# Kernel optimization log

Measured on AMD Instinct MI355X. Metric: run time of the kernel, lower is better.

The kernel has to match this reference:

```python
import jax, jax.numpy as jnp
import numpy as np
from jax import lax

T, H, W, HID, K = 128, 128, 128, 32, 3
DN = ('NCDHW', 'OIDHW', 'NCDHW')


def conv3dc(x, w, b=None, squeeze=False):
    # Conv3dC: 3D conv, kernel KxKxK, 'SAME' padding; return_squeezed drops channel dim
    y = lax.conv_general_dilated(x, w, (1, 1, 1), 'SAME', dimension_numbers=DN)
    if b is not None:
        y = y + b.reshape(1, -1, 1, 1, 1)
    if squeeze:
        y = jnp.squeeze(y, 1)
    return y


def setup_inputs() -> dict:
    key = jax.random.key(0)
    ks = jax.random.split(key, 10)
    X = jax.random.normal(ks[0], (1, T, H, W), dtype=jnp.float32)
    U = jax.random.normal(ks[1], (H * W, 1), dtype=jnp.float32) * 0.01
    V = jax.random.normal(ks[2], (1, T), dtype=jnp.float32) * 0.01
    M = jax.random.uniform(ks[3], (1, 1, T, H, W), dtype=jnp.float32)
    convM_w = jax.random.normal(ks[4], (HID, 1, K, K, K), dtype=jnp.float32) * 0.05
    conv0_w = jax.random.normal(ks[5], (1, HID, K, K, K), dtype=jnp.float32) * 0.05
    conv0_b = jnp.zeros((1,), dtype=jnp.float32)
    conv1_w = jax.random.normal(ks[6], (1, HID, K, K, K), dtype=jnp.float32) * 0.05
    conv2_w = jax.random.normal(ks[7], (HID, 1, K, K, K), dtype=jnp.float32) * 0.05
    conv4_w = jax.random.normal(ks[8], (1, HID, K, K, K), dtype=jnp.float32) * 0.05
    return {
        'X': X, 'U': U, 'V': V, 'M': M,
        'convM_w': convM_w, 'conv0_w': conv0_w, 'conv0_b': conv0_b,
        'conv1_w': conv1_w, 'conv2_w': conv2_w, 'conv4_w': conv4_w,
        'tau_s_raw': jnp.float32(1.0),
        'mask_scaling': jnp.float32(5.0),
        'g': jnp.ones((HID,), dtype=jnp.float32),
        'th': jnp.full((128,), 1.8, dtype=jnp.float32),
        'g2': jnp.ones((H,), dtype=jnp.float32),
        'u_learn2': jnp.ones((5,), dtype=jnp.float32),
        'v_learn2': jnp.ones((5,), dtype=jnp.float32),
    }


def reference(X, U, V, M, convM_w, conv0_w, conv0_b, conv1_w, conv2_w, conv4_w,
              tau_s_raw, mask_scaling, g, th, g2, u_learn2, v_learn2):
    tau_s = jax.nn.softplus(tau_s_raw)
    B, Td, Hd, Wd = X.shape
    Mh = conv3dc(M, convM_w)                                       # [1,HID,T,H,W]
    bg = 1.0 - jax.nn.relu(conv3dc(Mh, conv0_w, conv0_b, squeeze=True))  # [1,T,H,W]
    bg2 = jnp.square(bg)
    # 5-step unrolled rank-1 U/V gradient descent (faithful, incl. raw .view on (HW,T))
    for i in range(5):
        temp = bg2 * (X - jnp.reshape(U @ V, (1, Td, Hd, Wd)))
        temp = temp.reshape(Td, Hd * Wd)
        grad_U = temp.T @ V.T                                      # [HW,1]
        U = U + 1e-05 * u_learn2[i] * grad_U
        grad_V = (temp @ U).reshape(1, Td)                         # [1,T]
        V = V + 1e-05 * v_learn2[i] * grad_V
    L = (U @ V).T.reshape(Td, Hd, Wd)[None]                        # [1,T,H,W]
    fg2 = jnp.square(X - L)
    _X = tau_s * conv3dc((1.0 - conv3dc(Mh, conv1_w)) * fg2[:, None], conv2_w)
    Mtmp = Mh + _X                                                 # [1,HID,T,H,W]
    # soft_l1_reweighted2
    z = Mtmp.reshape(1, HID, Td, Hd * Wd)
    th2 = (th[None, None, :] * g2[None, :, None] * g[:, None, None]).reshape(HID, Hd * Wd)
    z = jnp.sign(z) * jax.nn.relu(jnp.abs(z) - th2[None, :, None, :])
    Mtmp = z.reshape(1, HID, Td, Hd, Wd)
    Mtmp = conv3dc(Mtmp, conv4_w, squeeze=True)                    # [1,T,H,W]
    M_out = jax.nn.sigmoid((Mtmp - 0.5) * mask_scaling)
    return (X, U, V, M_out)
```

## Files before the change

### kernel.cpp

```cpp
#include <hip/hip_runtime.h>
#include <math.h>

#define Tn 128
#define Hn 128
#define Wn 128
#define Cn 32
#define NVOX (Tn*Hn*Wn)

typedef float4 f4;
typedef unsigned short ushort_t;
typedef __attribute__((ext_vector_type(8))) short short8;
typedef __attribute__((ext_vector_type(4))) float f32x4;

__device__ __forceinline__ unsigned bfpack2(float a, float b) {
  unsigned ua = __float_as_uint(a), ub = __float_as_uint(b);
  ua = (ua + 0x7FFFu + ((ua >> 16) & 1u)) >> 16;
  ub = (ub + 0x7FFFu + ((ub >> 16) & 1u)) >> 16;
  return ua | (ub << 16);
}
__device__ __forceinline__ unsigned short bf1(float a) {
  unsigned u = __float_as_uint(a);
  u = (u + 0x7FFFu + ((u >> 16) & 1u)) >> 16;
  return (unsigned short)u;
}
__device__ __forceinline__ float bflo(unsigned p) { return __uint_as_float(p << 16); }
__device__ __forceinline__ float bfhi(unsigned p) { return __uint_as_float(p & 0xFFFF0000u); }
__device__ __forceinline__ float bfs(unsigned short s) { return __uint_as_float((unsigned)s << 16); }

union U4S8 { uint4 u; short8 s; };

__global__ __launch_bounds__(256) void k_convM(
    const float* __restrict__ M, const float* __restrict__ wM,
    uint4* __restrict__ Mh, const float* __restrict__ X,
    f4* __restrict__ outX)
{
  __shared__ float sm[1224];
  const int w0 = blockIdx.x*32, h0 = blockIdx.y*4, t0 = blockIdx.z*4;
  const int tid = threadIdx.x;
  const bool interior = (w0 != 0) && (w0 != 96) && (h0 != 0) && (h0 != 124)
                     && (t0 != 0) && (t0 != 124);
  for (int idx = tid; idx < 1224; idx += 256) {
    int lw = idx % 34, r = idx / 34, lh = r % 6, ld = r / 6;
    int gw = w0 - 1 + lw, gh = h0 - 1 + lh, gt = t0 - 1 + ld;
    float v = 0.f;
    if (interior || ((unsigned)gw < Wn && (unsigned)gh < Hn && (unsigned)gt < Tn))
      v = M[((long)gt*Hn + gh)*Wn + gw];
    sm[idx] = v;
  }
  const int bid = (blockIdx.z*32 + blockIdx.y)*4 + blockIdx.x;
  if (tid < 128) outX[bid*128 + tid] = ((const f4*)X)[bid*128 + tid];
  __syncthreads();

  const int wp = (tid & 15)*2, th = (tid>>4)&3, td = tid>>6;
  float2 m2[27];
  #pragma unroll
  for (int kd = 0; kd < 3; ++kd)
    #pragma unroll
    for (int kh = 0; kh < 3; ++kh) {
      const float* row = &sm[(((td+kd)*6) + (th+kh))*34 + wp];
      float2 a = *(const float2*)row;
      float2 b = *(const float2*)(row + 2);
      int k0 = (kd*3 + kh)*3;
      m2[k0+0] = make_float2(a.x, a.y);
      m2[k0+1] = make_float2(a.y, b.x);
      m2[k0+2] = make_float2(b.x, b.y);
    }
  const long vox = ((long)(t0+td)*Hn + (h0+th))*Wn + (w0+wp);
  uint4* dA = Mh + vox*4;
  uint4* dB = Mh + (vox+1)*4;
  #pragma unroll
  for (int j = 0; j < 4; ++j) {
    float rA[8], rB[8];
    #pragma unroll
    for (int e = 0; e < 8; ++e) {
      const int c = 8*j + e;
      float2 acc = {0.f, 0.f};
      #pragma unroll
      for (int k = 0; k < 27; ++k) {
        float wv = wM[c*27 + k];
        acc.x = fmaf(wv, m2[k].x, acc.x);
        acc.y = fmaf(wv, m2[k].y, acc.y);
      }
      rA[e] = acc.x; rB[e] = acc.y;
    }
    uint4 oA, oB;
    oA.x = bfpack2(rA[0],rA[1]); oA.y = bfpack2(rA[2],rA[3]);
    oA.z = bfpack2(rA[4],rA[5]); oA.w = bfpack2(rA[6],rA[7]);
    oB.x = bfpack2(rB[0],rB[1]); oB.y = bfpack2(rB[2],rB[3]);
    oB.z = bfpack2(rB[4],rB[5]); oB.w = bfpack2(rB[6],rB[7]);
    dA[j] = oA; dB[j] = oB;
  }
}

template<int S>
__device__ __forceinline__ auto& sel3(f32x4 (&a0)[4], f32x4 (&a1)[4], f32x4 (&a2)[4]) {
  if constexpr (S == 0) return a0;
  else if constexpr (S == 1) return a1;
  else return a2;
}

template<int KD>
__device__ __forceinline__ void kd_taps(
    const U4S8 (&A)[6][3], const uint4* sB, int bbase, int bstep,
    f32x4 (&acc)[4])
{
  const f32x4 fz = {0.f,0.f,0.f,0.f};
  #pragma unroll
  for (int kh = 0; kh < 3; ++kh)
    #pragma unroll
    for (int kw = 0; kw < 3; ++kw) {
      const int tap = KD*9 + kh*3 + kw;
      U4S8 b; b.u = sB[tap*bstep + bbase];
      const bool first = (KD == 0) && (kh == 0) && (kw == 0);
      #pragma unroll
      for (int lh = 0; lh < 4; ++lh)
        acc[lh] = __builtin_amdgcn_mfma_f32_16x16x32_bf16(
            A[lh+kh][kw].s, b.s, first ? fz : acc[lh], 0, 0, 0);
    }
}

template<int MODE, int P>
__device__ __forceinline__ void plane_step(
    const uint4* __restrict__ SRC, const uint4* sB,
    int tbase, int h0, int w0v, int lidx, int bbase, int bstep,
    int n, int kg, bool wL, bool wR, float scal,
    ushort_t* __restrict__ outH, float* __restrict__ outF,
    f32x4 (&a0)[4], f32x4 (&a1)[4], f32x4 (&a2)[4])
{
  const int gt = tbase - 1 + P;
  const bool tok = (unsigned)gt < Tn;
  U4S8 A[6][3];
  #pragma unroll
  for (int hr = 0; hr < 6; ++hr) {
    const int gh = h0 - 1 + hr;
    if (tok && (unsigned)gh < Hn) {
      const uint4* rowp = SRC + (((long)gt*Hn + gh)*Wn + (w0v - 1))*4;
      A[hr][0].u = rowp[lidx];
      A[hr][1].u = rowp[lidx + 4];
      A[hr][2].u = rowp[lidx + 8];
    } else {
      A[hr][0].u = (uint4){0u,0u,0u,0u};
      A[hr][1].u = (uint4){0u,0u,0u,0u};
      A[hr][2].u = (uint4){0u,0u,0u,0u};
    }
  }
  if (wL && n == 0) {
    #pragma unroll
    for (int hr = 0; hr < 6; ++hr) A[hr][0].u = (uint4){0u,0u,0u,0u};
  }
  if (wR && n == 15) {
    #pragma unroll
    for (int hr = 0; hr < 6; ++hr) A[hr][2].u = (uint4){0u,0u,0u,0u};
  }
  __builtin_amdgcn_sched_barrier(0);

  constexpr int kdlo = (P > 7) ? (P - 7) : 0;
  constexpr int kdhi = (P < 2) ? P : 2;
  if constexpr (0 >= kdlo && 0 <= kdhi)
    kd_taps<0>(A, sB, bbase, bstep, sel3<(P - 0) % 3>(a0, a1, a2));
  if constexpr (1 >= kdlo && 1 <= kdhi)
    kd_taps<1>(A, sB, bbase, bstep, sel3<(P - 1) % 3>(a0, a1, a2));
  if constexpr (2 >= kdlo && 2 <= kdhi)
    kd_taps<2>(A, sB, bbase, bstep, sel3<(P - 2) % 3>(a0, a1, a2));

  if constexpr (P >= 2) {
    constexpr int TR = P - 2;
    f32x4 (&acc)[4] = sel3<TR % 3>(a0, a1, a2);
    const int tt = tbase + TR;
    if constexpr (MODE == 0) {
      if (n < 2) {
        #pragma unroll
        for (int lh = 0; lh < 4; ++lh) {
          const long vbase = ((long)tt*Hn + (h0+lh))*Wn + w0v + kg*4;
          #pragma unroll
          for (int r = 0; r < 4; ++r) {
            float y = acc[lh][r];
            if (n == 0) { float bg = 1.f - fmaxf(y + scal, 0.f); outH[vbase+r] = bf1(bg*bg); }
            else        { outF[vbase+r] = 1.f - y; }
          }
        }
      }
    } else {
      if (n == 0) {
        #pragma unroll
        for (int lh = 0; lh < 4; ++lh) {
          const long vbase = ((long)tt*Hn + (h0+lh))*Wn + w0v + kg*4;
          #pragma unroll
          for (int r = 0; r < 4; ++r) {
            float y = (acc[lh][r] - 0.5f)*scal;
            outF[vbase+r] = 1.f/(1.f + expf(-y));
          }
        }
      }
    }
  }
}

template<int MODE>
__global__ __launch_bounds__(256, 2) void k_conv_fused(
    const uint4* __restrict__ SRC, const float* __restrict__ wAp,
    const float* __restrict__ wBp, const float* __restrict__ bias_or_ms,
    ushort_t* __restrict__ outH, float* __restrict__ outF)
{
  __shared__ uint4 sB[MODE == 0 ? 220 : 112];
  const int tid = threadIdx.x;
  const int lane = tid & 63;
  const int n = lane & 15, kg = lane >> 4;

  if constexpr (MODE == 0) {
    for (int idx = tid; idx < 220; idx += 256) {
      uint4 v = {0u,0u,0u,0u};
      if (idx < 216) {
        int tap = idx >> 3, col = (idx >> 2) & 1, kgi = idx & 3;
        const float* wp = col ? wBp : wAp;
        v.x = bfpack2(wp[(kgi*8+0)*27+tap], wp[(kgi*8+1)*27+tap]);
        v.y = bfpack2(wp[(kgi*8+2)*27+tap], wp[(kgi*8+3)*27+tap]);
        v.z = bfpack2(wp[(kgi*8+4)*27+tap], wp[(kgi*8+5)*27+tap]);
        v.w = bfpack2(wp[(kgi*8+6)*27+tap], wp[(kgi*8+7)*27+tap]);
      }
      sB[idx] = v;
    }
  } else {
    for (int idx = tid; idx < 112; idx += 256) {
      uint4 v = {0u,0u,0u,0u};
      if (idx < 108) {
        int tap = idx >> 2, kgi = idx & 3;
        v.x = bfpack2(wAp[(kgi*8+0)*27+tap], wAp[(kgi*8+1)*27+tap]);
        v.y = bfpack2(wAp[(kgi*8+2)*27+tap], wAp[(kgi*8+3)*27+tap]);
        v.z = bfpack2(wAp[(kgi*8+4)*27+tap], wAp[(kgi*8+5)*27+tap]);
        v.w = bfpack2(wAp[(kgi*8+6)*27+tap], wAp[(kgi*8+7)*27+tap]);
      }
      sB[idx] = v;
    }
  }
  const float scal = bias_or_ms[0];
  const int bbase = (MODE == 0) ? ((n < 2) ? (n*4 + kg) : (216 + kg))
                                : ((n == 0) ? kg : (108 + kg));
  const int bstep = (MODE == 0) ? ((n < 2) ? 8 : 0) : ((n == 0) ? 4 : 0);

  const int w0v = blockIdx.x*16, h0 = blockIdx.y*4;
  const int wv = __builtin_amdgcn_readfirstlane(tid >> 6);
  const int tbase = (blockIdx.z*4 + wv)*8;
  const int lidx = n*4 + kg;
  const bool wL = (w0v == 0), wR = (w0v == Wn-16);
  __syncthreads();

  f32x4 a0[4], a1[4], a2[4];

  #define PS(P) plane_step<MODE,P>(SRC, sB, tbase, h0, w0v, lidx, bbase, bstep, \
                                   n, kg, wL, wR, scal, outH, outF, a0, a1, a2);
  PS(0) PS(1) PS(2) PS(3) PS(4) PS(5) PS(6) PS(7) PS(8) PS(9)
  #undef PS
}

__global__ __launch_bounds__(512) void k_G(
    const float* __restrict__ X, const ushort_t* __restrict__ bg2h,
    const float* __restrict__ U0, const float* __restrict__ V0,
    float* __restrict__ G)
{
  __shared__ float Vs[128], Ucol[128], red[512];
  const int h = blockIdx.x;
  const int tid = threadIdx.x;
  const int w = tid & 127, tq = tid >> 7;
  if (tid < 128) Vs[tid] = V0[tid];
  else if (tid < 256) Ucol[tid-128] = U0[(tid-128)*128 + h];
  __syncthreads();
  const float vw = Vs[w];
  float acc = 0.f;
  const int tstart = tq*32;
  for (int t = tstart; t < tstart+32; ++t) {
    int idx = (t*Hn + h)*Wn + w;
    acc += bfs(bg2h[idx])*(X[idx] - Ucol[t]*vw)*Vs[t];
  }
  red[tid] = acc;
  __syncthreads();
  if (tq == 0)
    G[h*128 + w] = red[w] + red[128+w] + red[256+w] + red[384+w];
}

__global__ __launch_bounds__(256) void k_dotT(
    const float* __restrict__ X, const ushort_t* __restrict__ bg2h,
    const float* __restrict__ U0, const float* __restrict__ V0,
    const float* __restrict__ D, float* __restrict__ out)
{
  __shared__ float Uc[128], Vs[128], red[256];
  const int t = blockIdx.x, tid = threadIdx.x;
  if (tid < 128) { Uc[tid] = U0[t*128 + tid]; Vs[tid] = V0[tid]; }
  __syncthreads();
  float acc = 0.f;
  for (int idx = tid; idx < 16384; idx += 256) {
    int h = idx >> 7, w = idx & 127;
    int gi = t*16384 + idx;
    acc += bfs(bg2h[gi])*(X[gi] - Uc[h]*Vs[w])*D[idx];
  }
  red[tid] = acc;
  __syncthreads();
  for (int s = 128; s > 0; s >>= 1) {
    if (tid < s) red[tid] += red[tid+s];
    __syncthreads();
  }
  if (tid == 0) out[t] = red[0];
}

__global__ __launch_bounds__(256) void k_final(
    const float* __restrict__ U0, const float* __restrict__ V0,
    const float* __restrict__ G, const float* __restrict__ u1,
    const float* __restrict__ g2, const float* __restrict__ ul,
    const float* __restrict__ vl,
    float* __restrict__ Ua, float* __restrict__ Va,
    float* __restrict__ outU, float* __restrict__ outV)
{
  const int tid = threadIdx.x;
  float A = 0.f, cu1 = 0.f, cg2 = 0.f;
  #pragma unroll
  for (int i = 0; i < 5; ++i) {
    float ai = 1e-5f*ul[i], bi = 1e-5f*vl[i];
    A += ai; cu1 += bi; cg2 += bi*A;
  }
  for (int idx = tid; idx < 16384; idx += 256) {
    float u = U0[idx] + A*G[idx];
    Ua[idx] = u; outU[idx] = u;
  }
  if (tid < 128) {
    float v = V0[tid] + cu1*u1[tid] + cg2*g2[tid];
    Va[tid] = v; outV[tid] = v;
  }
}

__global__ __launch_bounds__(256, 2) void k_z(
    const float* __restrict__ X, const float* __restrict__ c1m,
    const float* __restrict__ Uf, const float* __restrict__ Vf,
    const float* __restrict__ w2, uint4* __restrict__ Mh,
    const float* __restrict__ taup, const float* __restrict__ g,
    const float* __restrict__ g2, const float* __restrict__ th)
{
  __shared__ float sm[1224];
  const int w0 = blockIdx.x*32, h0 = blockIdx.y*4, t0 = blockIdx.z*4;
  const int tid = threadIdx.x;

  const int wp = (tid & 15)*2, thl = (tid>>4)&3, td = tid>>6;
  const int h = h0 + thl, w = w0 + wp;
  const long vox = ((long)(t0+td)*Hn + h)*Wn + w;
  uint4* mA = Mh + vox*4;
  uint4* mB = Mh + (vox+1)*4;
  const uint4 pA0 = mA[0], pA1 = mA[1], pA2 = mA[2], pA3 = mA[3];
  const uint4 pB0 = mB[0], pB1 = mB[1], pB2 = mB[2], pB3 = mB[3];
  __builtin_amdgcn_sched_barrier(0);

  const bool interior = (w0 != 0) && (w0 != 96) && (h0 != 0) && (h0 != 124)
                     && (t0 != 0) && (t0 != 124);
  for (int idx = tid; idx < 1224; idx += 256) {
    int lw = idx % 34, r = idx / 34, lh = r % 6, ld = r / 6;
    int gw = w0 - 1 + lw, gh = h0 - 1 + lh, gt = t0 - 1 + ld;
    float qv = 0.f;
    if (interior || ((unsigned)gw < Wn && (unsigned)gh < Hn && (unsigned)gt < Tn)) {
      long gi = ((long)gt*Hn + gh)*Wn + gw;
      float d = X[gi] - Uf[gh*Wn + gw]*Vf[gt];
      qv = c1m[gi]*d*d;
    }
    sm[idx] = qv;
  }
  __syncthreads();

  const float tau_s = log1pf(expf(taup[0]));
  float2 m2[27];
  #pragma unroll
  for (int kd = 0; kd < 3; ++kd)
    #pragma unroll
    for (int kh = 0; kh < 3; ++kh) {
      const float* row = &sm[(((td+kd)*6) + (thl+kh))*34 + wp];
      float2 a = *(const float2*)row;
      float2 b = *(const float2*)(row + 2);
      int k0 = (kd*3 + kh)*3;
      m2[k0+0] = make_float2(a.x, a.y);
      m2[k0+1] = make_float2(a.y, b.x);
      m2[k0+2] = make_float2(b.x, b.y);
    }
  const float g2h = g2[h];
  const float thwA = g2h*th[w], thwB = g2h*th[w+1];

  #define ZJ(J, PA, PB)                                                     \
  {                                                                         \
    float inA[8] = {bflo(PA.x), bfhi(PA.x), bflo(PA.y), bfhi(PA.y),         \
                    bflo(PA.z), bfhi(PA.z), bflo(PA.w), bfhi(PA.w)};        \
    float inB[8] = {bflo(PB.x), bfhi(PB.x), bflo(PB.y), bfhi(PB.y),         \
                    bflo(PB.z), bfhi(PB.z), bflo(PB.w), bfhi(PB.w)};        \
    float oA[8], oB[8];                                                     \
    _Pragma("unroll")                                                       \
    for (int e = 0; e < 8; ++e) {                                           \
      const int c = 8*(J) + e;                                              \
      float2 acc = {0.f, 0.f};                                              \
      _Pragma("unroll")                                                     \
      for (int k = 0; k < 27; ++k) {                                        \
        float wv = w2[c*27 + k];                                            \
        acc.x = fmaf(wv, m2[k].x, acc.x);                                   \
        acc.y = fmaf(wv, m2[k].y, acc.y);                                   \
      }                                                                     \
      float gc = g[c];                                                      \
      float rA = inA[e] + tau_s*acc.x;                                      \
      float aA = fabsf(rA) - gc*thwA;                                       \
      oA[e] = (aA > 0.f) ? copysignf(aA, rA) : 0.f;                         \
      float rB = inB[e] + tau_s*acc.y;                                      \
      float aB = fabsf(rB) - gc*thwB;                                       \
      oB[e] = (aB > 0.f) ? copysignf(aB, rB) : 0.f;                         \
    }                                                                       \
    uint4 qA, qB;                                                           \
    qA.x = bfpack2(oA[0],oA[1]); qA.y = bfpack2(oA[2],oA[3]);               \
    qA.z = bfpack2(oA[4],oA[5]); qA.w = bfpack2(oA[6],oA[7]);               \
    qB.x = bfpack2(oB[0],oB[1]); qB.y = bfpack2(oB[2],oB[3]);               \
    qB.z = bfpack2(oB[4],oB[5]); qB.w = bfpack2(oB[6],oB[7]);               \
    mA[J] = qA; mB[J] = qB;                                                 \
  }

  ZJ(0, pA0, pB0)
  ZJ(1, pA1, pB1)
  ZJ(2, pA2, pB2)
  ZJ(3, pA3, pB3)
  #undef ZJ
}

extern "C" void kernel_launch(void* const* d_in, const int* in_sizes, int n_in,
                              void* d_out, int out_size, void* d_ws, size_t ws_size,
                              hipStream_t stream)
{
  const float* X   = (const float*)d_in[0];
  const float* U0  = (const float*)d_in[1];
  const float* V0  = (const float*)d_in[2];
  const float* M   = (const float*)d_in[3];
  const float* wM  = (const float*)d_in[4];
  const float* w0  = (const float*)d_in[5];
  const float* b0  = (const float*)d_in[6];
  const float* w1  = (const float*)d_in[7];
  const float* w2  = (const float*)d_in[8];
  const float* w4  = (const float*)d_in[9];
  const float* tau = (const float*)d_in[10];
  const float* ms  = (const float*)d_in[11];
  const float* g   = (const float*)d_in[12];
  const float* th  = (const float*)d_in[13];
  const float* g2  = (const float*)d_in[14];
  const float* ul  = (const float*)d_in[15];
  const float* vl  = (const float*)d_in[16];

  float*    c1m  = (float*)d_ws;
  uint4*    Mh   = (uint4*)((char*)d_ws + (size_t)NVOX*4);
  ushort_t* bg2h = (ushort_t*)((char*)Mh + (size_t)NVOX*64);
  float*    Ua   = (float*)((char*)bg2h + (size_t)NVOX*2);
  float*    Va   = Ua + 16384;
  float*    G    = Va + 128;
  float*    u1   = G + 16384;
  float*    g2v  = u1 + 128;

  float* out_f  = (float*)d_out;
  f4*    outX   = (f4*)d_out;
  float* outU   = out_f + NVOX;
  float* outV   = outU + 16384;
  float* outM   = outV + 128;

  k_convM <<<dim3(4,32,32), 256, 0, stream>>>(M, wM, Mh, X, outX);
  k_conv_fused<0><<<dim3(8,32,4), 256, 0, stream>>>(Mh, w0, w1, b0, bg2h, c1m);

  k_G    <<<128, 512, 0, stream>>>(X, bg2h, U0, V0, G);
  k_dotT <<<128, 256, 0, stream>>>(X, bg2h, U0, V0, U0, u1);
  k_dotT <<<128, 256, 0, stream>>>(X, bg2h, U0, V0, G, g2v);
  k_final<<<1, 256, 0, stream>>>(U0, V0, G, u1, g2v, ul, vl, Ua, Va, outU, outV);

  k_z    <<<dim3(4,32,32), 256, 0, stream>>>(X, c1m, Ua, Va, w2, Mh,
                                             tau, g, g2, th);
  k_conv_fused<1><<<dim3(8,32,4), 256, 0, stream>>>(Mh, w4, w4, ms, nullptr, outM);
}
```

Before: 449.4 us.

## Double-buffer plane loads in MFMA conv, pack FMAs, raise k_z occupancy

The MFMA conv kernel now splits each plane step into a load phase and an MFMA/retire phase, ping-ponging two A register buffers so the next plane's global loads are issued while the current plane's MFMAs run. k_convM switches its scalar FMA pairs to a two-wide vector FMA so the compiler can emit packed FMA instructions. k_z raises its launch-bounds occupancy hint from 2 to 4 blocks and moves the Mh prefetch after the shared-memory fill to cut live registers. Together these aim to hide memory latency and raise throughput, at the cost of higher register pressure in the conv kernel and possible spills in k_z.

```diff
diff --git a/kernel.cpp b/kernel.cpp
--- a/kernel.cpp
+++ b/kernel.cpp
@@ -11,6 +11,7 @@
 typedef unsigned short ushort_t;
 typedef __attribute__((ext_vector_type(8))) short short8;
 typedef __attribute__((ext_vector_type(4))) float f32x4;
+typedef __attribute__((ext_vector_type(2))) float f32x2;
 
 __device__ __forceinline__ unsigned bfpack2(float a, float b) {
   unsigned ua = __float_as_uint(a), ub = __float_as_uint(b);
@@ -26,6 +27,11 @@
 __device__ __forceinline__ float bflo(unsigned p) { return __uint_as_float(p << 16); }
 __device__ __forceinline__ float bfhi(unsigned p) { return __uint_as_float(p & 0xFFFF0000u); }
 __device__ __forceinline__ float bfs(unsigned short s) { return __uint_as_float((unsigned)s << 16); }
+
+__device__ __forceinline__ f32x2 pfma(f32x2 a, float b, f32x2 c) {
+  f32x2 bb = {b, b};
+  return __builtin_elementwise_fma(a, bb, c);
+}
 
 union U4S8 { uint4 u; short8 s; };
 
@@ -52,7 +58,7 @@
   __syncthreads();
 
   const int wp = (tid & 15)*2, th = (tid>>4)&3, td = tid>>6;
-  float2 m2[27];
+  f32x2 m2[27];
   #pragma unroll
   for (int kd = 0; kd < 3; ++kd)
     #pragma unroll
@@ -61,9 +67,9 @@
       float2 a = *(const float2*)row;
       float2 b = *(const float2*)(row + 2);
       int k0 = (kd*3 + kh)*3;
-      m2[k0+0] = make_float2(a.x, a.y);
-      m2[k0+1] = make_float2(a.y, b.x);
-      m2[k0+2] = make_float2(b.x, b.y);
+      m2[k0+0] = (f32x2){a.x, a.y};
+      m2[k0+1] = (f32x2){a.y, b.x};
+      m2[k0+2] = (f32x2){b.x, b.y};
     }
   const long vox = ((long)(t0+td)*Hn + (h0+th))*Wn + (w0+wp);
   uint4* dA = Mh + vox*4;
@@ -74,13 +80,10 @@
     #pragma unroll
     for (int e = 0; e < 8; ++e) {
       const int c = 8*j + e;
-      float2 acc = {0.f, 0.f};
+      f32x2 acc = {0.f, 0.f};
       #pragma unroll
-      for (int k = 0; k < 27; ++k) {
-        float wv = wM[c*27 + k];
-        acc.x = fmaf(wv, m2[k].x, acc.x);
-        acc.y = fmaf(wv, m2[k].y, acc.y);
-      }
+      for (int k = 0; k < 27; ++k)
+        acc = pfma(m2[k], wM[c*27 + k], acc);
       rA[e] = acc.x; rB[e] = acc.y;
     }
     uint4 oA, oB;
@@ -99,37 +102,13 @@
   else return a2;
 }
 
-template<int KD>
-__device__ __forceinline__ void kd_taps(
-    const U4S8 (&A)[6][3], const uint4* sB, int bbase, int bstep,
-    f32x4 (&acc)[4])
-{
-  const f32x4 fz = {0.f,0.f,0.f,0.f};
-  #pragma unroll
-  for (int kh = 0; kh < 3; ++kh)
-    #pragma unroll
-    for (int kw = 0; kw < 3; ++kw) {
-      const int tap = KD*9 + kh*3 + kw;
-      U4S8 b; b.u = sB[tap*bstep + bbase];
-      const bool first = (KD == 0) && (kh == 0) && (kw == 0);
-      #pragma unroll
-      for (int lh = 0; lh < 4; ++lh)
-        acc[lh] = __builtin_amdgcn_mfma_f32_16x16x32_bf16(
-            A[lh+kh][kw].s, b.s, first ? fz : acc[lh], 0, 0, 0);
-    }
-}
-
-template<int MODE, int P>
-__device__ __forceinline__ void plane_step(
-    const uint4* __restrict__ SRC, const uint4* sB,
-    int tbase, int h0, int w0v, int lidx, int bbase, int bstep,
-    int n, int kg, bool wL, bool wR, float scal,
-    ushort_t* __restrict__ outH, float* __restrict__ outF,
-    f32x4 (&a0)[4], f32x4 (&a1)[4], f32x4 (&a2)[4])
+template<int P>
+__device__ __forceinline__ void load_plane(
+    const uint4* __restrict__ SRC, int tbase, int h0, int w0v, int lidx,
+    int n, bool wL, bool wR, U4S8 (&A)[6][3])
 {
   const int gt = tbase - 1 + P;
   const bool tok = (unsigned)gt < Tn;
-  U4S8 A[6][3];
   #pragma unroll
   for (int hr = 0; hr < 6; ++hr) {
     const int gh = h0 - 1 + hr;
@@ -152,8 +131,36 @@
     #pragma unroll
     for (int hr = 0; hr < 6; ++hr) A[hr][2].u = (uint4){0u,0u,0u,0u};
   }
-  __builtin_amdgcn_sched_barrier(0);
-
+}
+
+template<int KD>
+__device__ __forceinline__ void kd_taps(
+    const U4S8 (&A)[6][3], const uint4* sB, int bbase, int bstep,
+    f32x4 (&acc)[4])
+{
+  const f32x4 fz = {0.f,0.f,0.f,0.f};
+  #pragma unroll
+  for (int kh = 0; kh < 3; ++kh)
+    #pragma unroll
+    for (int kw = 0; kw < 3; ++kw) {
+      const int tap = KD*9 + kh*3 + kw;
+      U4S8 b; b.u = sB[tap*bstep + bbase];
+      const bool first = (KD == 0) && (kh == 0) && (kw == 0);
+      #pragma unroll
+      for (int lh = 0; lh < 4; ++lh)
+        acc[lh] = __builtin_amdgcn_mfma_f32_16x16x32_bf16(
+            A[lh+kh][kw].s, b.s, first ? fz : acc[lh], 0, 0, 0);
+    }
+}
+
+template<int MODE, int P>
+__device__ __forceinline__ void mfma_retire(
+    const uint4* sB, const U4S8 (&A)[6][3],
+    int tbase, int h0, int w0v, int bbase, int bstep,
+    int n, int kg, float scal,
+    ushort_t* __restrict__ outH, float* __restrict__ outF,
+    f32x4 (&a0)[4], f32x4 (&a1)[4], f32x4 (&a2)[4])
+{
   constexpr int kdlo = (P > 7) ? (P - 7) : 0;
   constexpr int kdhi = (P < 2) ? P : 2;
   if constexpr (0 >= kdlo && 0 <= kdhi)
@@ -246,11 +253,28 @@
   __syncthreads();
 
   f32x4 a0[4], a1[4], a2[4];
-
-  #define PS(P) plane_step<MODE,P>(SRC, sB, tbase, h0, w0v, lidx, bbase, bstep, \
-                                   n, kg, wL, wR, scal, outH, outF, a0, a1, a2);
-  PS(0) PS(1) PS(2) PS(3) PS(4) PS(5) PS(6) PS(7) PS(8) PS(9)
-  #undef PS
+  U4S8 Aa[6][3], Ab[6][3];
+
+  #define PL(P, AR) load_plane<P>(SRC, tbase, h0, w0v, lidx, n, wL, wR, AR);
+  #define PM(P, AR) mfma_retire<MODE,P>(sB, AR, tbase, h0, w0v, bbase, bstep, \
+                                        n, kg, scal, outH, outF, a0, a1, a2);
+  #define SB __builtin_amdgcn_sched_barrier(0);
+
+  PL(0, Aa) PL(1, Ab) SB
+  PM(0, Aa) PL(2, Aa) SB
+  PM(1, Ab) PL(3, Ab) SB
+  PM(2, Aa) PL(4, Aa) SB
+  PM(3, Ab) PL(5, Ab) SB
+  PM(4, Aa) PL(6, Aa) SB
+  PM(5, Ab) PL(7, Ab) SB
+  PM(6, Aa) PL(8, Aa) SB
+  PM(7, Ab) PL(9, Ab) SB
+  PM(8, Aa) SB
+  PM(9, Ab)
+
+  #undef PL
+  #undef PM
+  #undef SB
 }
 
 __global__ __launch_bounds__(512) void k_G(
@@ -327,7 +351,7 @@
   }
 }
 
-__global__ __launch_bounds__(256, 2) void k_z(
+__global__ __launch_bounds__(256, 4) void k_z(
     const float* __restrict__ X, const float* __restrict__ c1m,
     const float* __restrict__ Uf, const float* __restrict__ Vf,
     const float* __restrict__ w2, uint4* __restrict__ Mh,
@@ -337,16 +361,6 @@
   __shared__ float sm[1224];
   const int w0 = blockIdx.x*32, h0 = blockIdx.y*4, t0 = blockIdx.z*4;
   const int tid = threadIdx.x;
-
-  const int wp = (tid & 15)*2, thl = (tid>>4)&3, td = tid>>6;
-  const int h = h0 + thl, w = w0 + wp;
-  const long vox = ((long)(t0+td)*Hn + h)*Wn + w;
-  uint4* mA = Mh + vox*4;
-  uint4* mB = Mh + (vox+1)*4;
-  const uint4 pA0 = mA[0], pA1 = mA[1], pA2 = mA[2], pA3 = mA[3];
-  const uint4 pB0 = mB[0], pB1 = mB[1], pB2 = mB[2], pB3 = mB[3];
-  __builtin_amdgcn_sched_barrier(0);
-
   const bool interior = (w0 != 0) && (w0 != 96) && (h0 != 0) && (h0 != 124)
                      && (t0 != 0) && (t0 != 124);
   for (int idx = tid; idx < 1224; idx += 256) {
@@ -361,6 +375,17 @@
     sm[idx] = qv;
   }
   __syncthreads();
+
+  const int wp = (tid & 15)*2, thl = (tid>>4)&3, td = tid>>6;
+  const int h = h0 + thl, w = w0 + wp;
+  const long vox = ((long)(t0+td)*Hn + h)*Wn + w;
+  uint4* mA = Mh + vox*4;
+  uint4* mB = Mh + (vox+1)*4;
+  const uint4 pA0 = mA[0], pB0 = mB[0];
+  const uint4 pA1 = mA[1], pB1 = mB[1];
+  const uint4 pA2 = mA[2], pB2 = mB[2];
+  const uint4 pA3 = mA[3], pB3 = mB[3];
+  __builtin_amdgcn_sched_barrier(0);
 
   const float tau_s = log1pf(expf(taup[0]));
   float2 m2[27];
```

New measurement: 441.9 us. No clear change (-1.7%).
